# Kernel optimization log

Measured on AMD Instinct MI355X. Metric: run time of the kernel, lower is better.

## Reference

```python
import jax, jax.numpy as jnp
import numpy as np

EMBED_DIM = 512
NUM_HEADS = 8
HEAD_DIM = EMBED_DIM // NUM_HEADS


def setup_inputs() -> dict:
    key = jax.random.key(0)
    ks = jax.random.split(key, 5)
    B, N, D = 2, 4096, EMBED_DIM
    s_in = 1.0 / np.sqrt(D)
    x = jax.random.normal(ks[0], (B, N, D), dtype=jnp.float32)
    qkv_w = jax.random.uniform(ks[1], (3 * D, D), dtype=jnp.float32, minval=-s_in, maxval=s_in)
    qkv_b = jax.random.uniform(ks[2], (3 * D,), dtype=jnp.float32, minval=-s_in, maxval=s_in)
    out_w = jax.random.uniform(ks[3], (D, D), dtype=jnp.float32, minval=-s_in, maxval=s_in)
    out_b = jax.random.uniform(ks[4], (D,), dtype=jnp.float32, minval=-s_in, maxval=s_in)
    return {"x": x, "qkv_w": qkv_w, "qkv_b": qkv_b, "out_w": out_w, "out_b": out_b}


def reference(x, qkv_w, qkv_b, out_w, out_b):
    B, N, D = x.shape
    H, Hd = NUM_HEADS, HEAD_DIM
    # qkv projection: [B,N,3D] -> [3,B,H,N,Hd]
    qkv = x @ qkv_w.T + qkv_b
    qkv = qkv.reshape(B, N, 3, H, Hd).transpose(2, 0, 3, 1, 4)
    q, k, v = qkv[0], qkv[1], qkv[2]
    scale = 1.0 / jnp.sqrt(jnp.asarray(Hd, dtype=x.dtype))
    scores = jnp.einsum("bhnd,bhmd->bhnm", q, k) * scale  # [B,H,N,N]
    weights = jax.nn.softmax(scores, axis=-1)
    out = jnp.einsum("bhnm,bhmd->bhnd", weights, v)  # [B,H,N,Hd]
    out = out.transpose(0, 2, 1, 3).reshape(B, N, D)
    return out @ out_w.T + out_b
```

## Files before the change

### kernel.cpp

```cpp
#include <hip/hip_runtime.h>

typedef __attribute__((ext_vector_type(8))) short short8;
typedef __attribute__((ext_vector_type(2))) float f32x2;
typedef __attribute__((ext_vector_type(4))) float f32x4;
typedef __attribute__((ext_vector_type(16))) float f32x16;
typedef unsigned short u16;
typedef unsigned int u32;

#define SCQ 0.18033688011112042f

__device__ __forceinline__ u16 f2b(float f) {
  unsigned u = __builtin_bit_cast(unsigned, f);
  u += 0x7FFFu + ((u >> 16) & 1u);
  return (u16)(u >> 16);
}

__device__ __forceinline__ u32 cvtpk(float a, float b) {
  u32 r;
  asm("v_cvt_pk_bf16_f32 %0, %1, %2" : "=v"(r) : "v"(a), "v"(b));
  return r;
}

__device__ __forceinline__ float ex2(float x) { return __builtin_amdgcn_exp2f(x); }

__device__ __forceinline__ void gl_lds16(const u16* g, u16* l) {
  __builtin_amdgcn_global_load_lds(
      (const __attribute__((address_space(1))) unsigned int*)g,
      (__attribute__((address_space(3))) unsigned int*)l, 16, 0, 0);
}

__global__ __launch_bounds__(256) void convert_k(
    const float* __restrict__ x, const float* __restrict__ w1, const float* __restrict__ w2,
    u16* __restrict__ xb, u16* __restrict__ w1b, u16* __restrict__ w2b) {
  const int NXv = (8192 * 512) / 4;
  const int NW1v = (1536 * 512) / 4;
  const int NW2v = (512 * 512) / 4;
  int i = blockIdx.x * 256 + threadIdx.x;
  const float4* src;
  u16* dst;
  int j;
  float scale = 1.0f;
  if (i < NXv) {
    src = (const float4*)x; dst = xb; j = i;
  } else if (i < NXv + NW1v) {
    j = i - NXv; src = (const float4*)w1; dst = w1b;
    if (j < (512 * 512) / 4) scale = SCQ;
  } else {
    j = i - NXv - NW1v;
    if (j >= NW2v) return;
    src = (const float4*)w2; dst = w2b;
  }
  float4 v = src[j];
  ushort4 o;
  o.x = f2b(v.x * scale); o.y = f2b(v.y * scale);
  o.z = f2b(v.z * scale); o.w = f2b(v.w * scale);
  *reinterpret_cast<ushort4*>(dst + (size_t)j * 4) = o;
}

__global__ __launch_bounds__(256) void qkv_gemm(
    const u16* __restrict__ Ab, const u16* __restrict__ Bw, const float* __restrict__ bias,
    u16* __restrict__ Qd, u16* __restrict__ Kd, u16* __restrict__ Vtd) {
  const int m0 = blockIdx.x * 128, n0 = blockIdx.y * 128;
  const int tid = threadIdx.x, wave = tid >> 6, lane = tid & 63;
  const int g = lane >> 4, lr = lane & 15;
  const int wm = (wave >> 1) * 64, wn = (wave & 1) * 64;
  __shared__ alignas(16) u16 Al[128 * 64];
  __shared__ alignas(16) u16 Bl[128 * 64];

  f32x4 acc[4][4];
#pragma unroll
  for (int mf = 0; mf < 4; ++mf)
#pragma unroll
    for (int nf = 0; nf < 4; ++nf)
#pragma unroll
      for (int r = 0; r < 4; ++r) acc[mf][nf][r] = 0.0f;

  const int gid0 = wave * 64 + lane;

  for (int k0 = 0; k0 < 512; k0 += 64) {
    __syncthreads();
#pragma unroll
    for (int c = 0; c < 4; ++c) {
      const int gid = c * 256 + gid0;
      const int row = gid >> 3;
      const int col = ((gid & 7) ^ (row & 7)) << 3;
      gl_lds16(Ab + (size_t)(m0 + row) * 512 + k0 + col, Al + (size_t)(c * 256 + wave * 64) * 8);
      gl_lds16(Bw + (size_t)(n0 + row) * 512 + k0 + col, Bl + (size_t)(c * 256 + wave * 64) * 8);
    }
    __syncthreads();
#pragma unroll
    for (int kb = 0; kb < 2; ++kb) {
      short8 bf[4], af[4];
#pragma unroll
      for (int nf = 0; nf < 4; ++nf)
        bf[nf] = *reinterpret_cast<const short8*>(
            Bl + (wn + nf * 16 + lr) * 64 + (((kb * 4 + g) ^ (lr & 7)) << 3));
#pragma unroll
      for (int mf = 0; mf < 4; ++mf)
        af[mf] = *reinterpret_cast<const short8*>(
            Al + (wm + mf * 16 + lr) * 64 + (((kb * 4 + g) ^ (lr & 7)) << 3));
#pragma unroll
      for (int mf = 0; mf < 4; ++mf)
#pragma unroll
        for (int nf = 0; nf < 4; ++nf)
          acc[mf][nf] = __builtin_amdgcn_mfma_f32_16x16x32_bf16(af[mf], bf[nf], acc[mf][nf], 0, 0, 0);
    }
  }
#pragma unroll
  for (int mf = 0; mf < 4; ++mf)
#pragma unroll
    for (int nf = 0; nf < 4; ++nf)
#pragma unroll
      for (int r = 0; r < 4; ++r) {
        int row = m0 + wm + mf * 16 + g * 4 + r;
        int col = n0 + wn + nf * 16 + lr;
        float bv = bias[col];
        if (col < 512) bv *= SCQ;
        u16 val = f2b(acc[mf][nf][r] + bv);
        int which = col >> 9, dcol = col & 511;
        int h = dcol >> 6, hd = dcol & 63;
        int b = row >> 12, n = row & 4095;
        size_t hb = (size_t)(b * 8 + h);
        if (which == 0)      Qd[(hb * 4096 + n) * 64 + hd] = val;
        else if (which == 1) Kd[(hb * 4096 + n) * 64 + hd] = val;
        else                 Vtd[(hb * 64 + hd) * 4096 + n] = val;
      }
}

__global__ __launch_bounds__(256, 2) void attn13(
    const u16* __restrict__ Qd, const u16* __restrict__ Kd, const u16* __restrict__ Vtd,
    float* __restrict__ Op, float* __restrict__ Lp) {
  int f = blockIdx.x;
  int xcd = f & 7, slot = f >> 3;
  int bh = (xcd << 1) + (slot >> 5);
  int rem = slot & 31;
  int half = rem >> 4;
  int qb = rem & 15;

  const int tid = threadIdx.x, wave = tid >> 6, lane = tid & 63;
  const int hi = lane >> 5, lq = lane & 31;

  const u16* Qh = Qd + (size_t)bh * (4096 * 64);
  const u16* Kh = Kd + (size_t)bh * (4096 * 64);
  const u16* Vh = Vtd + (size_t)bh * (64 * 4096);
  float* Oh = Op + (size_t)half * (8192 * 512);
  float* Lh = Lp + (size_t)half * (16 * 4096);

  __shared__ alignas(16) u16 Kl[2][128 * 64];

  const int qrow_base = qb * 256 + wave * 64;

  short8 qf[2][4];
#pragma unroll
  for (int qt = 0; qt < 2; ++qt)
#pragma unroll
    for (int s = 0; s < 4; ++s)
      qf[qt][s] = *reinterpret_cast<const short8*>(
          Qh + (size_t)(qrow_base + qt * 32 + lq) * 64 + s * 16 + hi * 8);

  f32x16 acc[2][2];
#pragma unroll
  for (int qt = 0; qt < 2; ++qt)
#pragma unroll
    for (int dt = 0; dt < 2; ++dt)
#pragma unroll
      for (int i = 0; i < 16; ++i) acc[qt][dt][i] = 0.0f;

  f32x16 Z;
#pragma unroll
  for (int i = 0; i < 16; ++i) Z[i] = 0.0f;

  float lrun[2] = {0.0f, 0.0f};

  const int kv0 = half * 2048;
  const int gid0 = wave * 64 + lane;

#pragma unroll
  for (int c = 0; c < 4; ++c) {
    const int gid = c * 256 + gid0;
    const int row = gid >> 3;
    const int col = ((gid & 7) ^ (row & 7)) << 3;
    gl_lds16(Kh + (size_t)(kv0 + row) * 64 + col, &Kl[0][(c * 256 + wave * 64) * 8]);
  }
  __syncthreads();

  f32x16 stA0, stA1, stB0, stB1;
  short8 vfA[2][2], vfB[2][2];
  short8 pbA0[2], pbA1[2], pbB0[2], pbB1[2];

#define QK_HALF(st0, st1, h)                                                        \
  {                                                                                 \
    const int rb = ((h) * 32 + lq) * 64;                                            \
    __builtin_amdgcn_s_setprio(1);                                                  \
    _Pragma("unroll")                                                               \
    for (int s = 0; s < 4; ++s) {                                                   \
      const int ch = ((2 * s + hi) ^ (lq & 7)) << 3;                                \
      short8 kf = *reinterpret_cast<const short8*>(&Kl[cur][rb + ch]);              \
      if (s == 0) {                                                                 \
        st0 = __builtin_amdgcn_mfma_f32_32x32x16_bf16(kf, qf[0][0], Z, 0, 0, 0);    \
        st1 = __builtin_amdgcn_mfma_f32_32x32x16_bf16(kf, qf[1][0], Z, 0, 0, 0);    \
      } else {                                                                      \
        st0 = __builtin_amdgcn_mfma_f32_32x32x16_bf16(kf, qf[0][s], st0, 0, 0, 0);  \
        st1 = __builtin_amdgcn_mfma_f32_32x32x16_bf16(kf, qf[1][s], st1, 0, 0, 0);  \
      }                                                                             \
    }                                                                               \
    __builtin_amdgcn_s_setprio(0);                                                  \
  }

#define LOADV_HALF(vf, h)                                                           \
  {                                                                                 \
    const int off = kbase + (h) * 32 + hi * 8;                                      \
    vf[0][0] = *reinterpret_cast<const short8*>(Vh + (size_t)lq * 4096 + off);      \
    vf[0][1] = *reinterpret_cast<const short8*>(Vh + (size_t)(32 + lq) * 4096 + off); \
    vf[1][0] = *reinterpret_cast<const short8*>(Vh + (size_t)lq * 4096 + off + 16); \
    vf[1][1] = *reinterpret_cast<const short8*>(Vh + (size_t)(32 + lq) * 4096 + off + 16); \
  }

#define SM_QT(stq, pbq, qt_idx)                                                     \
  {                                                                                 \
    f32x2 p2[8];                                                                    \
    _Pragma("unroll")                                                               \
    for (int j = 0; j < 8; ++j) {                                                   \
      p2[j][0] = ex2(stq[2 * j]);                                                   \
      p2[j][1] = ex2(stq[2 * j + 1]);                                               \
    }                                                                               \
    f32x2 s0 = (p2[0] + p2[1]) + (p2[2] + p2[3]);                                   \
    f32x2 s1 = (p2[4] + p2[5]) + (p2[6] + p2[7]);                                   \
    f32x2 sm = s0 + s1;                                                             \
    lrun[qt_idx] += sm[0] + sm[1];                                                  \
    _Pragma("unroll")                                                               \
    for (int t = 0; t < 2; ++t) {                                                   \
      u32 wa = cvtpk(p2[4 * t + 0][0], p2[4 * t + 0][1]);                           \
      u32 wb = cvtpk(p2[4 * t + 2][0], p2[4 * t + 2][1]);                           \
      u32 wc = cvtpk(p2[4 * t + 1][0], p2[4 * t + 1][1]);                           \
      u32 wd = cvtpk(p2[4 * t + 3][0], p2[4 * t + 3][1]);                           \
      asm volatile("v_permlane32_swap_b32 %0, %1" : "+v"(wa), "+v"(wb));            \
      asm volatile("v_permlane32_swap_b32 %0, %1" : "+v"(wc), "+v"(wd));            \
      int4 wv;                                                                      \
      wv.x = (int)wa; wv.y = (int)wc; wv.z = (int)wb; wv.w = (int)wd;               \
      pbq[t] = __builtin_bit_cast(short8, wv);                                      \
    }                                                                               \
  }

#define PV_HALF(vf, pb0, pb1)                                                       \
  {                                                                                 \
    __builtin_amdgcn_s_setprio(1);                                                  \
    _Pragma("unroll")                                                               \
    for (int t = 0; t < 2; ++t) {                                                   \
      acc[0][0] = __builtin_amdgcn_mfma_f32_32x32x16_bf16(vf[t][0], pb0[t], acc[0][0], 0, 0, 0); \
      acc[0][1] = __builtin_amdgcn_mfma_f32_32x32x16_bf16(vf[t][1], pb0[t], acc[0][1], 0, 0, 0); \
      acc[1][0] = __builtin_amdgcn_mfma_f32_32x32x16_bf16(vf[t][0], pb1[t], acc[1][0], 0, 0, 0); \
      acc[1][1] = __builtin_amdgcn_mfma_f32_32x32x16_bf16(vf[t][1], pb1[t], acc[1][1], 0, 0, 0); \
    }                                                                               \
    __builtin_amdgcn_s_setprio(0);                                                  \
  }

#pragma unroll 1
  for (int kt = 0; kt < 16; ++kt) {
    const int cur = kt & 1;
    const int kbase = kv0 + kt * 128;

    if (kt + 1 < 16) {
      const u16* kn = Kh + (size_t)(kbase + 128) * 64;
#pragma unroll
      for (int c = 0; c < 4; ++c) {
        const int gid = c * 256 + gid0;
        const int row = gid >> 3;
        const int col = ((gid & 7) ^ (row & 7)) << 3;
        gl_lds16(kn + (size_t)row * 64 + col, &Kl[cur ^ 1][(c * 256 + wave * 64) * 8]);
      }
    }

    QK_HALF(stA0, stA1, 0);
    LOADV_HALF(vfA, 0);
#pragma unroll
    for (int hp = 0; hp < 2; ++hp) {
      const int h = hp * 2;
      QK_HALF(stB0, stB1, h + 1);
      LOADV_HALF(vfB, h + 1);
      SM_QT(stA0, pbA0, 0);
      SM_QT(stA1, pbA1, 1);
      PV_HALF(vfA, pbA0, pbA1);
      if (hp == 0) {
        QK_HALF(stA0, stA1, h + 2);
        LOADV_HALF(vfA, h + 2);
      }
      SM_QT(stB0, pbB0, 0);
      SM_QT(stB1, pbB1, 1);
      PV_HALF(vfB, pbB0, pbB1);
    }

    __syncthreads();
  }
#undef QK_HALF
#undef LOADV_HALF
#undef SM_QT
#undef PV_HALF

  const int b = bh >> 3, h = bh & 7;
#pragma unroll
  for (int qt = 0; qt < 2; ++qt) {
    const int qn = qrow_base + qt * 32 + lq;
    const size_t rowoff = ((size_t)(b * 4096 + qn)) * 512 + h * 64;
#pragma unroll
    for (int dt = 0; dt < 2; ++dt)
#pragma unroll
      for (int t = 0; t < 4; ++t) {
        f32x4 v4;
        v4[0] = acc[qt][dt][4 * t + 0];
        v4[1] = acc[qt][dt][4 * t + 1];
        v4[2] = acc[qt][dt][4 * t + 2];
        v4[3] = acc[qt][dt][4 * t + 3];
        *reinterpret_cast<f32x4*>(Oh + rowoff + dt * 32 + t * 8 + hi * 4) = v4;
      }
    float lt = lrun[qt] + __shfl_xor(lrun[qt], 32);
    if (hi == 0) Lh[(bh << 12) + qn] = lt;
  }
}

__global__ __launch_bounds__(256) void combine_k(
    const float* __restrict__ Op, const float* __restrict__ Lp,
    u16* __restrict__ attnb) {
  int idx = blockIdx.x * 256 + threadIdx.x;
  int row = idx >> 7, c4 = idx & 127;
  int b = row >> 12, n = row & 4095, h = c4 >> 4;
  int li = (((b << 3) + h) << 12) + n;
  float l = Lp[li] + Lp[li + 65536];
  float inv = 1.0f / l;
  const int STRIDE = 8192 * 512 / 4;
  float4 o0 = reinterpret_cast<const float4*>(Op)[idx];
  float4 o1 = reinterpret_cast<const float4*>(Op)[idx + STRIDE];
  ushort4 o;
  o.x = f2b((o0.x + o1.x) * inv);
  o.y = f2b((o0.y + o1.y) * inv);
  o.z = f2b((o0.z + o1.z) * inv);
  o.w = f2b((o0.w + o1.w) * inv);
  *reinterpret_cast<ushort4*>(attnb + (size_t)idx * 4) = o;
}

__global__ __launch_bounds__(256) void out_gemm(
    const u16* __restrict__ Ab, const u16* __restrict__ Bw, const float* __restrict__ bias,
    float* __restrict__ out) {
  const int m0 = blockIdx.x * 128, n0 = blockIdx.y * 64;
  const int tid = threadIdx.x, wave = tid >> 6, lane = tid & 63;
  const int g = lane >> 4, lr = lane & 15;
  const int wm = (wave >> 1) * 64, wn = (wave & 1) * 32;
  __shared__ alignas(16) u16 Al[128][72];
  __shared__ alignas(16) u16 Bl[64][72];

  f32x4 acc[4][2];
#pragma unroll
  for (int mf = 0; mf < 4; ++mf)
#pragma unroll
    for (int nf = 0; nf < 2; ++nf)
#pragma unroll
      for (int r = 0; r < 4; ++r) acc[mf][nf][r] = 0.0f;

  const int rr = tid >> 3, cc = tid & 7;
  for (int k0 = 0; k0 < 512; k0 += 64) {
    __syncthreads();
#pragma unroll
    for (int it = 0; it < 4; ++it)
      *reinterpret_cast<short8*>(&Al[rr + it * 32][cc * 8]) =
          *reinterpret_cast<const short8*>(Ab + (size_t)(m0 + rr + it * 32) * 512 + k0 + cc * 8);
#pragma unroll
    for (int it = 0; it < 2; ++it)
      *reinterpret_cast<short8*>(&Bl[rr + it * 32][cc * 8]) =
          *reinterpret_cast<const short8*>(Bw + (size_t)(n0 + rr + it * 32) * 512 + k0 + cc * 8);
    __syncthreads();
#pragma unroll
    for (int kb = 0; kb < 2; ++kb) {
      short8 bf[2], af[4];
#pragma unroll
      for (int nf = 0; nf < 2; ++nf)
        bf[nf] = *reinterpret_cast<const short8*>(&Bl[wn + nf * 16 + lr][kb * 32 + g * 8]);
#pragma unroll
      for (int mf = 0; mf < 4; ++mf)
        af[mf] = *reinterpret_cast<const short8*>(&Al[wm + mf * 16 + lr][kb * 32 + g * 8]);
#pragma unroll
      for (int mf = 0; mf < 4; ++mf)
#pragma unroll
        for (int nf = 0; nf < 2; ++nf)
          acc[mf][nf] = __builtin_amdgcn_mfma_f32_16x16x32_bf16(af[mf], bf[nf], acc[mf][nf], 0, 0, 0);
    }
  }
#pragma unroll
  for (int mf = 0; mf < 4; ++mf)
#pragma unroll
    for (int nf = 0; nf < 2; ++nf)
#pragma unroll
      for (int r = 0; r < 4; ++r) {
        int row = m0 + wm + mf * 16 + g * 4 + r;
        int col = n0 + wn + nf * 16 + lr;
        out[(size_t)row * 512 + col] = acc[mf][nf][r] + bias[col];
      }
}

extern "C" void kernel_launch(void* const* d_in, const int* in_sizes, int n_in,
                              void* d_out, int out_size, void* d_ws, size_t ws_size,
                              hipStream_t stream) {
  const float* x = (const float*)d_in[0];
  const float* qkv_w = (const float*)d_in[1];
  const float* qkv_b = (const float*)d_in[2];
  const float* out_w = (const float*)d_in[3];
  const float* out_b = (const float*)d_in[4];
  float* out = (float*)d_out;

  char* ws = (char*)d_ws;
  u16* xb    = (u16*)(ws + 0);
  u16* w1b   = (u16*)(ws + 8388608);
  u16* w2b   = (u16*)(ws + 9961472);
  u16* Qd    = (u16*)(ws + 10485760);
  u16* Kd    = (u16*)(ws + 18874368);
  u16* Vtd   = (u16*)(ws + 27262976);
  u16* attnb = (u16*)(ws + 35651584);
  float* Op  = (float*)(ws + 44040192);
  float* Lp  = (float*)(ws + 77594624);

  convert_k<<<5120, 256, 0, stream>>>(x, qkv_w, out_w, xb, w1b, w2b);
  qkv_gemm<<<dim3(64, 12), 256, 0, stream>>>(xb, w1b, qkv_b, Qd, Kd, Vtd);
  attn13<<<512, 256, 0, stream>>>(Qd, Kd, Vtd, Op, Lp);
  combine_k<<<4096, 256, 0, stream>>>(Op, Lp, attnb);
  out_gemm<<<dim3(64, 8), 256, 0, stream>>>(attnb, w2b, out_b, out);
}
```

Baseline: 141.0 us.

## Give each wave a private K tile in LDS, removing block barriers

```diff
diff --git a/kernel.cpp b/kernel.cpp
--- a/kernel.cpp
+++ b/kernel.cpp
@@ -127,7 +127,7 @@
       }
 }
 
-__global__ __launch_bounds__(256, 2) void attn13(
+__global__ __launch_bounds__(256, 2) void attn14(
     const u16* __restrict__ Qd, const u16* __restrict__ Kd, const u16* __restrict__ Vtd,
     float* __restrict__ Op, float* __restrict__ Lp) {
   int f = blockIdx.x;
@@ -146,7 +146,7 @@
   float* Oh = Op + (size_t)half * (8192 * 512);
   float* Lh = Lp + (size_t)half * (16 * 4096);
 
-  __shared__ alignas(16) u16 Kl[2][128 * 64];
+  __shared__ alignas(16) u16 Kl[4][2][64 * 64];
 
   const int qrow_base = qb * 256 + wave * 64;
 
@@ -173,29 +173,30 @@
   float lrun[2] = {0.0f, 0.0f};
 
   const int kv0 = half * 2048;
-  const int gid0 = wave * 64 + lane;
-
-#pragma unroll
-  for (int c = 0; c < 4; ++c) {
-    const int gid = c * 256 + gid0;
-    const int row = gid >> 3;
-    const int col = ((gid & 7) ^ (row & 7)) << 3;
-    gl_lds16(Kh + (size_t)(kv0 + row) * 64 + col, &Kl[0][(c * 256 + wave * 64) * 8]);
-  }
-  __syncthreads();
+
+  const int soff = ((lane >> 3) * 64) + ((((lane & 7) ^ ((lane >> 3) & 7))) << 3);
+
+#define STAGE_TILE(buf, kptr)                                          \
+  {                                                                    \
+    const u16* s_ = (kptr) + soff;                                     \
+    u16* d_ = &Kl[wave][buf][0];                                       \
+    _Pragma("unroll")                                                  \
+    for (int c = 0; c < 8; ++c) gl_lds16(s_ + c * 512, d_ + c * 512);  \
+  }
+
+  STAGE_TILE(0, Kh + (size_t)kv0 * 64);
 
   f32x16 stA0, stA1, stB0, stB1;
   short8 vfA[2][2], vfB[2][2];
   short8 pbA0[2], pbA1[2], pbB0[2], pbB1[2];
 
-#define QK_HALF(st0, st1, h)                                                        \
+#define QK_HALF(st0, st1, h, kl)                                                    \
   {                                                                                 \
-    const int rb = ((h) * 32 + lq) * 64;                                            \
     __builtin_amdgcn_s_setprio(1);                                                  \
     _Pragma("unroll")                                                               \
     for (int s = 0; s < 4; ++s) {                                                   \
       const int ch = ((2 * s + hi) ^ (lq & 7)) << 3;                                \
-      short8 kf = *reinterpret_cast<const short8*>(&Kl[cur][rb + ch]);              \
+      short8 kf = *reinterpret_cast<const short8*>(&(kl)[((h) * 32 + lq) * 64 + ch]); \
       if (s == 0) {                                                                 \
         st0 = __builtin_amdgcn_mfma_f32_32x32x16_bf16(kf, qf[0][0], Z, 0, 0, 0);    \
         st1 = __builtin_amdgcn_mfma_f32_32x32x16_bf16(kf, qf[1][0], Z, 0, 0, 0);    \
@@ -256,42 +257,29 @@
   }
 
 #pragma unroll 1
-  for (int kt = 0; kt < 16; ++kt) {
+  for (int kt = 0; kt < 32; ++kt) {
     const int cur = kt & 1;
-    const int kbase = kv0 + kt * 128;
-
-    if (kt + 1 < 16) {
-      const u16* kn = Kh + (size_t)(kbase + 128) * 64;
-#pragma unroll
-      for (int c = 0; c < 4; ++c) {
-        const int gid = c * 256 + gid0;
-        const int row = gid >> 3;
-        const int col = ((gid & 7) ^ (row & 7)) << 3;
-        gl_lds16(kn + (size_t)row * 64 + col, &Kl[cur ^ 1][(c * 256 + wave * 64) * 8]);
-      }
-    }
-
-    QK_HALF(stA0, stA1, 0);
+    const int kbase = kv0 + kt * 64;
+    const u16* kl = &Kl[wave][cur][0];
+
+    asm volatile("s_waitcnt vmcnt(0)" ::: "memory");
+
+    QK_HALF(stA0, stA1, 0, kl);
+    QK_HALF(stB0, stB1, 1, kl);
+
     LOADV_HALF(vfA, 0);
-#pragma unroll
-    for (int hp = 0; hp < 2; ++hp) {
-      const int h = hp * 2;
-      QK_HALF(stB0, stB1, h + 1);
-      LOADV_HALF(vfB, h + 1);
-      SM_QT(stA0, pbA0, 0);
-      SM_QT(stA1, pbA1, 1);
-      PV_HALF(vfA, pbA0, pbA1);
-      if (hp == 0) {
-        QK_HALF(stA0, stA1, h + 2);
-        LOADV_HALF(vfA, h + 2);
-      }
-      SM_QT(stB0, pbB0, 0);
-      SM_QT(stB1, pbB1, 1);
-      PV_HALF(vfB, pbB0, pbB1);
-    }
-
-    __syncthreads();
-  }
+    LOADV_HALF(vfB, 1);
+
+    if (kt + 1 < 32) STAGE_TILE(cur ^ 1, Kh + (size_t)(kbase + 64) * 64);
+
+    SM_QT(stA0, pbA0, 0);
+    SM_QT(stA1, pbA1, 1);
+    PV_HALF(vfA, pbA0, pbA1);
+    SM_QT(stB0, pbB0, 0);
+    SM_QT(stB1, pbB1, 1);
+    PV_HALF(vfB, pbB0, pbB1);
+  }
+#undef STAGE_TILE
 #undef QK_HALF
 #undef LOADV_HALF
 #undef SM_QT
@@ -419,7 +407,7 @@
 
   convert_k<<<5120, 256, 0, stream>>>(x, qkv_w, out_w, xb, w1b, w2b);
   qkv_gemm<<<dim3(64, 12), 256, 0, stream>>>(xb, w1b, qkv_b, Qd, Kd, Vtd);
-  attn13<<<512, 256, 0, stream>>>(Qd, Kd, Vtd, Op, Lp);
+  attn14<<<512, 256, 0, stream>>>(Qd, Kd, Vtd, Op, Lp);
   combine_k<<<4096, 256, 0, stream>>>(Op, Lp, attnb);
   out_gemm<<<dim3(64, 8), 256, 0, stream>>>(attnb, w2b, out_b, out);
 }
```

Measured after the change: 153.7 us. +9.0%, slower.
